# Kernel tuning notes

Hardware: AMD Instinct MI355X
Metric: run time of the kernel (lower is better)

The kernel has to match this reference:

```python
import jax, jax.numpy as jnp
import numpy as np

DIM = 128
HEAD_K = 4
EXPAND = DIM * HEAD_K  # 512
B, H, W = 16, 32, 32


def setup_inputs() -> dict:
    key = jax.random.key(0)
    ks = jax.random.split(key, 6)
    s = 0.05
    return {
        "x": jax.random.normal(ks[0], (B, DIM, H, W), dtype=jnp.float32),
        "Wq": jax.random.normal(ks[1], (EXPAND, DIM), dtype=jnp.float32) * s,
        "Wk": jax.random.normal(ks[2], (EXPAND, DIM), dtype=jnp.float32) * s,
        "Wv": jax.random.normal(ks[3], (EXPAND, DIM), dtype=jnp.float32) * s,
        "bv": jnp.zeros((EXPAND,), dtype=jnp.float32),
        "Wt": jax.random.normal(ks[4], (DIM, EXPAND), dtype=jnp.float32) * s,
        "bt": jnp.zeros((DIM,), dtype=jnp.float32),
    }


def reference(x, Wq, Wk, Wv, bv, Wt, bt):
    b, c, h, w = x.shape
    hw = h * w
    norm = jnp.asarray(c ** 0.5, x.dtype)
    xf = x.reshape(b, c, hw)  # 1x1 conv == channel matmul
    # [B, expand, HW] -> [B, head_k, dim, HW]
    q = jnp.einsum('oc,bcn->bon', Wq, xf).reshape(b, HEAD_K, DIM, hw)
    k = jnp.einsum('oc,bcn->bon', Wk, xf).reshape(b, HEAD_K, DIM, hw)
    v = (jnp.einsum('oc,bcn->bon', Wv, xf) + bv[None, :, None]).reshape(b, HEAD_K, DIM, hw)
    # score: [B, head_k, HW, HW]
    score = jax.nn.softmax(jnp.einsum('bhdn,bhdm->bhnm', q, k) / norm, axis=-1)
    # weighted sum: [B, head_k, HW, dim] -> reshape (row-major) to [B, expand, H, W]
    wsv = jnp.einsum('bhnm,bhdm->bhnd', score, v).reshape(b, HEAD_K * DIM, h, w)
    # BaseConv transform: residual + 1x1 conv projection back to dim
    proj = jnp.einsum('oc,bcn->bon', Wt, wsv.reshape(b, HEAD_K * DIM, hw)) + bt[None, :, None]
    return x + proj.reshape(b, c, h, w)
```

## Files before the change

### kernel.cpp

```cpp
#include <hip/hip_runtime.h>
#include <hip/hip_bf16.h>


#define NB 16
#define CD 128
#define HWN 1024
#define NH 4
#define KVB 64

typedef __attribute__((ext_vector_type(8))) short bf16x8;
typedef __attribute__((ext_vector_type(4))) short bf16x4;
typedef __attribute__((ext_vector_type(4))) float f32x4;
typedef __attribute__((ext_vector_type(16))) float f32x16;

static __device__ __forceinline__ short f2bf(float f) {
  union { float f; unsigned u; } v; v.f = f;
  unsigned r = v.u + 0x7fffu + ((v.u >> 16) & 1u);
  return (short)(r >> 16);
}

static __device__ __forceinline__ unsigned pk2(float a, float b) {
  unsigned r;
  asm("v_cvt_pk_bf16_f32 %0, %1, %2" : "=v"(r) : "v"(a), "v"(b));
  return r;
}

static __device__ __forceinline__ bf16x4 pk4(float a0, float a1, float a2, float a3) {
  union { unsigned u[2]; bf16x4 s; } r;
  r.u[0] = pk2(a0, a1);
  r.u[1] = pk2(a2, a3);
  return r.s;
}

#define PSWAP(a, b) asm("v_permlane32_swap_b32 %0, %1" : "+v"(a), "+v"(b))

static __device__ __forceinline__ float xswap32(float x, int lane) {
  union { float f; unsigned u; } a, b;
  a.f = x; b.f = x;
  PSWAP(a.u, b.u);
  return (lane < 32) ? b.f : a.f;
}

__global__ void prep(const float* __restrict__ x, const float* __restrict__ Wq,
                     const float* __restrict__ Wk, const float* __restrict__ Wv,
                     const float* __restrict__ Wt,
                     short* __restrict__ wqkv, short* __restrict__ wtb,
                     short* __restrict__ xt) {
  __shared__ short tile[32][33];
  if (blockIdx.z == 16) {
    const float SC = 0.08838834764831845f * 1.44269504088896341f;
    int gid = (blockIdx.x * 4 + blockIdx.y) * 256 + threadIdx.x;
#pragma unroll
    for (int t = 0; t < 2; ++t) {
      int i = gid + t * 32768;
      wqkv[i]          = f2bf(Wq[i] * SC);
      wqkv[i + 65536]  = f2bf(Wk[i]);
      wqkv[i + 131072] = f2bf(Wv[i]);
      wtb[i]           = f2bf(Wt[i]);
    }
    return;
  }
  int b = blockIdx.z, c0 = blockIdx.y * 32, n0 = blockIdx.x * 32;
  int tx = threadIdx.x & 31, ty = threadIdx.x >> 5;
  const float* xp = x + ((size_t)b * CD + c0) * HWN + n0;
  for (int k = 0; k < 4; ++k)
    tile[ty + 8 * k][tx] = f2bf(xp[(size_t)(ty + 8 * k) * HWN + tx]);
  __syncthreads();
  short* xo = xt + ((size_t)b * HWN + n0) * CD + c0;
  for (int k = 0; k < 4; ++k)
    xo[(size_t)(ty + 8 * k) * CD + tx] = tile[tx][ty + 8 * k];
}

__launch_bounds__(256)
__global__ void qkv_gemm(const short* __restrict__ wqkv, const short* __restrict__ xt,
                         const float* __restrict__ bv,
                         short* __restrict__ Qt, short* __restrict__ Kt,
                         short* __restrict__ Vd) {
  int b = blockIdx.z;
  int wave = threadIdx.x >> 6, lane = threadIdx.x & 63;
  int l15 = lane & 15, l4 = lane >> 4;
  int o0 = blockIdx.y * 128 + wave * 32;
  int n0 = blockIdx.x * 128;
  bool isV = (blockIdx.y >= 8);

  bf16x8 afrag[2][4];
  for (int of = 0; of < 2; ++of)
    for (int kt = 0; kt < 4; ++kt)
      afrag[of][kt] = *(const bf16x8*)(wqkv + (size_t)(o0 + of * 16 + l15) * CD + kt * 32 + l4 * 8);

  f32x4 acc[2][8];
  for (int of = 0; of < 2; ++of)
    for (int jt = 0; jt < 8; ++jt) acc[of][jt] = (f32x4){0.f, 0.f, 0.f, 0.f};

  const short* xb = xt + (size_t)b * HWN * CD;
  if (!isV) {
    for (int jt = 0; jt < 8; ++jt) {
      int n = n0 + jt * 16 + l15;
      for (int kt = 0; kt < 4; ++kt) {
        bf16x8 bfrag = *(const bf16x8*)(xb + (size_t)n * CD + kt * 32 + l4 * 8);
        acc[0][jt] = __builtin_amdgcn_mfma_f32_16x16x32_bf16(afrag[0][kt], bfrag, acc[0][jt], 0, 0, 0);
        acc[1][jt] = __builtin_amdgcn_mfma_f32_16x16x32_bf16(afrag[1][kt], bfrag, acc[1][jt], 0, 0, 0);
      }
    }
    short* dst = (o0 < 512) ? Qt : Kt;
    int oo = (o0 < 512) ? o0 : o0 - 512;
    for (int of = 0; of < 2; ++of) {
      int h = (oo + of * 16) >> 7, d0 = ((oo + of * 16) & 127) + l4 * 4;
      for (int jt = 0; jt < 8; ++jt) {
        int n = n0 + jt * 16 + l15;
        *(bf16x4*)(dst + (((size_t)b * NH + h) * HWN + n) * CD + d0) =
            pk4(acc[of][jt][0], acc[of][jt][1], acc[of][jt][2], acc[of][jt][3]);
      }
    }
  } else {
    for (int jt = 0; jt < 8; ++jt) {
      int n = n0 + jt * 16 + l15;
      for (int kt = 0; kt < 4; ++kt) {
        bf16x8 bfrag = *(const bf16x8*)(xb + (size_t)n * CD + kt * 32 + l4 * 8);
        acc[0][jt] = __builtin_amdgcn_mfma_f32_16x16x32_bf16(bfrag, afrag[0][kt], acc[0][jt], 0, 0, 0);
        acc[1][jt] = __builtin_amdgcn_mfma_f32_16x16x32_bf16(bfrag, afrag[1][kt], acc[1][jt], 0, 0, 0);
      }
    }
    int oo = o0 - 1024;
    for (int of = 0; of < 2; ++of) {
      int h = (oo + of * 16) >> 7, dr = ((oo + of * 16) & 127) + l15;
      float bvl = bv[oo + of * 16 + l15];
      for (int jt = 0; jt < 8; ++jt) {
        *(bf16x4*)(Vd + (((size_t)b * NH + h) * CD + dr) * HWN + n0 + jt * 16 + l4 * 4) =
            pk4(acc[of][jt][0] + bvl, acc[of][jt][1] + bvl,
                acc[of][jt][2] + bvl, acc[of][jt][3] + bvl);
      }
    }
  }
}

__launch_bounds__(256, 2)
__global__ void attn(const short* __restrict__ Qt, const short* __restrict__ Kt,
                     const short* __restrict__ Vd, short* __restrict__ Oscr) {
  int wid = blockIdx.x;
  int work = (wid & 7) * 64 + (wid >> 3);
  int xb = work & 7;
  int h = (work >> 3) & 3;
  int b = work >> 5;

  int wave = threadIdx.x >> 6, lane = threadIdx.x & 63;
  int l15 = lane & 15, l4 = lane >> 4;
  int q5 = lane & 31, hi = lane >> 5;
  int n0 = xb * 128 + wave * 32;
  size_t bh = (size_t)b * NH + h;
  const short* q = Qt + bh * HWN * CD;
  const short* k = Kt + bh * HWN * CD;
  const short* v = Vd + bh * CD * HWN;

  __shared__ short Kls[2][KVB * CD];
  __shared__ short Vls[2][CD * KVB];

#define STAGE(buf, m0s)                                                         \
  for (int j = 0; j < 4; ++j) {                                                 \
    int ii = wave * 4 + j;                                                      \
    int krow = ii * 4 + l4;                                                     \
    int kcol = (l15 * 16) ^ ((krow & 7) << 4);                                  \
    const short* kgp = k + (size_t)((m0s) + krow) * CD + (kcol >> 1);           \
    __builtin_amdgcn_global_load_lds(                                           \
        (const __attribute__((address_space(1))) void*)kgp,                     \
        (__attribute__((address_space(3))) void*)&Kls[buf][ii * 512], 16, 0, 0);\
    int vrow = ii * 8 + (lane >> 3);                                            \
    int vcol = ((lane & 7) * 16) ^ ((vrow & 7) << 4);                           \
    const short* vgp = v + (size_t)vrow * HWN + (m0s) + (vcol >> 1);            \
    __builtin_amdgcn_global_load_lds(                                           \
        (const __attribute__((address_space(1))) void*)vgp,                     \
        (__attribute__((address_space(3))) void*)&Vls[buf][ii * 512], 16, 0, 0);\
  }

  bf16x8 bq[8];
  for (int kt = 0; kt < 8; ++kt)
    bq[kt] = *(const bf16x8*)(q + (size_t)(n0 + q5) * CD + kt * 16 + hi * 8);

  f32x16 oacc[4];
  for (int dt = 0; dt < 4; ++dt)
#pragma unroll
    for (int r = 0; r < 16; ++r) oacc[dt][r] = 0.f;
  float mi = -1e30f, li = 0.f;

  STAGE(0, 0)
  __syncthreads();

  for (int mt = 0; mt < 16; ++mt) {
    int m0 = mt * KVB;
    int cur = mt & 1;
    if (mt < 15) STAGE(cur ^ 1, m0 + KVB)

    f32x16 s0, s1;
#pragma unroll
    for (int r = 0; r < 16; ++r) { s0[r] = 0.f; s1[r] = 0.f; }
    __builtin_amdgcn_s_setprio(1);
#pragma unroll
    for (int kt = 0; kt < 8; ++kt) {
      int col = kt * 16 + hi * 8;
      bf16x8 ak0 = *(const bf16x8*)&Kls[cur][q5 * CD + (col ^ ((q5 & 7) << 3))];
      bf16x8 ak1 = *(const bf16x8*)&Kls[cur][(32 + q5) * CD + (col ^ ((q5 & 7) << 3))];
      s0 = __builtin_amdgcn_mfma_f32_32x32x16_bf16(ak0, bq[kt], s0, 0, 0, 0);
      s1 = __builtin_amdgcn_mfma_f32_32x32x16_bf16(ak1, bq[kt], s1, 0, 0, 0);
    }
    __builtin_amdgcn_s_setprio(0);

    float mx = s0[0];
#pragma unroll
    for (int r = 1; r < 16; ++r) mx = fmaxf(mx, s0[r]);
#pragma unroll
    for (int r = 0; r < 16; ++r) mx = fmaxf(mx, s1[r]);
    mx = fmaxf(mx, xswap32(mx, lane));

    if (!__all(mx - mi <= 8.0f)) {
      float nm = fmaxf(mi, mx);
      float fac = __builtin_amdgcn_exp2f(mi - nm);
      mi = nm;
      li *= fac;
      for (int dt = 0; dt < 4; ++dt)
#pragma unroll
        for (int r = 0; r < 16; ++r) oacc[dt][r] *= fac;
    }
    float ls = 0.f;
#pragma unroll
    for (int r = 0; r < 16; ++r) {
      float e0 = __builtin_amdgcn_exp2f(s0[r] - mi);
      float e1 = __builtin_amdgcn_exp2f(s1[r] - mi);
      s0[r] = e0; s1[r] = e1;
      ls += e0 + e1;
    }
    ls += xswap32(ls, lane);
    li += ls;

    unsigned pkw[2][4][2];
#pragma unroll
    for (int g = 0; g < 4; ++g) {
      pkw[0][g][0] = pk2(s0[4 * g + 0], s0[4 * g + 1]);
      pkw[0][g][1] = pk2(s0[4 * g + 2], s0[4 * g + 3]);
      pkw[1][g][0] = pk2(s1[4 * g + 0], s1[4 * g + 1]);
      pkw[1][g][1] = pk2(s1[4 * g + 2], s1[4 * g + 3]);
    }
    bf16x8 pb[4];
#pragma unroll
    for (int ks = 0; ks < 4; ++ks) {
      int t = ks >> 1, G0 = 2 * (ks & 1);
      unsigned a0 = pkw[t][G0][0], b0 = pkw[t][G0 + 1][0];
      unsigned a1 = pkw[t][G0][1], b1 = pkw[t][G0 + 1][1];
      PSWAP(a0, b0);
      PSWAP(a1, b1);
      union { unsigned u[4]; bf16x8 v; } f;
      f.u[0] = a0; f.u[1] = a1; f.u[2] = b0; f.u[3] = b1;
      pb[ks] = f.v;
    }

    __builtin_amdgcn_s_setprio(1);
#pragma unroll
    for (int dt = 0; dt < 4; ++dt) {
      int d = dt * 32 + q5;
      const short* vb = &Vls[cur][d * KVB];
#pragma unroll
      for (int ks = 0; ks < 4; ++ks) {
        bf16x8 av = *(const bf16x8*)&vb[(ks * 16 + hi * 8) ^ ((d & 7) << 3)];
        oacc[dt] = __builtin_amdgcn_mfma_f32_32x32x16_bf16(av, pb[ks], oacc[dt], 0, 0, 0);
      }
    }
    __builtin_amdgcn_s_setprio(0);

    __syncthreads();
  }
#undef STAGE

  float inv = 1.0f / li;
  int n = n0 + q5;
  int o = h * CD + (n >> 3);
  size_t base = ((size_t)b * HWN + (n & 7) * CD) * 512 + o;
  for (int dt = 0; dt < 4; ++dt) {
#pragma unroll
    for (int r = 0; r < 16; ++r) {
      int d = dt * 32 + (r & 3) + 8 * (r >> 2) + 4 * hi;
      Oscr[base + (size_t)d * 512] = f2bf(oacc[dt][r] * inv);
    }
  }
}

__launch_bounds__(256)
__global__ void proj_kernel(const short* __restrict__ Oscr, const short* __restrict__ wtb,
                            const float* __restrict__ bt, const float* __restrict__ x,
                            float* __restrict__ out) {
  int b = blockIdx.y;
  int wave = threadIdx.x >> 6, lane = threadIdx.x & 63;
  int l15 = lane & 15, l4 = lane >> 4;
  int m0 = blockIdx.x * 32 + (wave & 1) * 16;
  int c0 = (wave >> 1) * 64;

  f32x4 acc[4];
  for (int jt = 0; jt < 4; ++jt) acc[jt] = (f32x4){0.f, 0.f, 0.f, 0.f};

  const short* ob = Oscr + (size_t)b * HWN * 512;
  for (int kt = 0; kt < 16; ++kt) {
    bf16x8 a = *(const bf16x8*)(ob + (size_t)(m0 + l15) * 512 + kt * 32 + l4 * 8);
    for (int jt = 0; jt < 4; ++jt) {
      bf16x8 bw = *(const bf16x8*)(wtb + (size_t)(c0 + jt * 16 + l15) * 512 + kt * 32 + l4 * 8);
      acc[jt] = __builtin_amdgcn_mfma_f32_16x16x32_bf16(a, bw, acc[jt], 0, 0, 0);
    }
  }
  for (int jt = 0; jt < 4; ++jt) {
    int c = c0 + jt * 16 + l15;
    float btc = bt[c];
    size_t base = ((size_t)b * CD + c) * HWN + m0 + l4 * 4;
    f32x4 xr = *(const f32x4*)(x + base);
    f32x4 o;
    for (int r = 0; r < 4; ++r) o[r] = acc[jt][r] + xr[r] + btc;
    *(f32x4*)(out + base) = o;
  }
}

extern "C" void kernel_launch(void* const* d_in, const int* in_sizes, int n_in,
                              void* d_out, int out_size, void* d_ws, size_t ws_size,
                              hipStream_t stream) {
  const float* x  = (const float*)d_in[0];
  const float* Wq = (const float*)d_in[1];
  const float* Wk = (const float*)d_in[2];
  const float* Wv = (const float*)d_in[3];
  const float* bv = (const float*)d_in[4];
  const float* Wt = (const float*)d_in[5];
  const float* bt = (const float*)d_in[6];
  float* out = (float*)d_out;
  char* ws = (char*)d_ws;

  short* wqkv = (short*)(ws);
  short* wtb  = (short*)(ws + 393216);
  short* xt   = (short*)(ws + 524288);
  short* Qt   = (short*)(ws + 4718592);
  short* Kt   = (short*)(ws + 21495808);
  short* Vd   = (short*)(ws + 38273024);
  short* Oscr = (short*)(ws + 55050240);

  hipLaunchKernelGGL(prep, dim3(32, 4, 17), dim3(256), 0, stream, x, Wq, Wk, Wv, Wt, wqkv, wtb, xt);
  hipLaunchKernelGGL(qkv_gemm, dim3(8, 12, 16), dim3(256), 0, stream, wqkv, xt, bv, Qt, Kt, Vd);
  hipLaunchKernelGGL(attn, dim3(512), dim3(256), 0, stream, Qt, Kt, Vd, Oscr);
  hipLaunchKernelGGL(proj_kernel, dim3(32, 16), dim3(256), 0, stream, Oscr, wtb, bt, x, out);
}
```

Measured before the change: 115.7 us.

## Stage GEMM operand tiles in swizzled LDS via direct loads, remap blocks per XCD

The qkv and projection GEMMs now load their shared activation tile (xt rows or Oscr rows) once per block into XOR-swizzled LDS using global_load_lds. Before, each wave re-read those rows from global memory. Both kernels move to a 1D grid with a work remap that groups batches across the 8 XCDs to improve L2 locality. s_setprio raises priority around the MFMA loops. The cost is extra LDS per block (32 KB) and a barrier, which may limit occupancy.

Result: faster. 100.8 us (-12.9%).

```diff
diff --git a/kernel.cpp b/kernel.cpp
--- a/kernel.cpp
+++ b/kernel.cpp
@@ -76,12 +76,30 @@
                          const float* __restrict__ bv,
                          short* __restrict__ Qt, short* __restrict__ Kt,
                          short* __restrict__ Vd) {
-  int b = blockIdx.z;
+  int wid = blockIdx.x;
+  int work = (wid & 7) * 192 + (wid >> 3);
+  int b = work / 96;
+  int rem = work - b * 96;
+  int oy = rem >> 3;
+  int nx = rem & 7;
+
   int wave = threadIdx.x >> 6, lane = threadIdx.x & 63;
   int l15 = lane & 15, l4 = lane >> 4;
-  int o0 = blockIdx.y * 128 + wave * 32;
-  int n0 = blockIdx.x * 128;
-  bool isV = (blockIdx.y >= 8);
+  int o0 = oy * 128 + wave * 32;
+  int n0 = nx * 128;
+  bool isV = (oy >= 8);
+
+  __shared__ short Xls[128 * CD];
+
+  for (int j = 0; j < 8; ++j) {
+    int ii = wave * 8 + j;
+    int row = ii * 4 + l4;
+    int scol = (l15 * 16) ^ ((row & 7) << 4);
+    const short* gp = xt + ((size_t)b * HWN + n0 + row) * CD + (scol >> 1);
+    __builtin_amdgcn_global_load_lds(
+        (const __attribute__((address_space(1))) void*)gp,
+        (__attribute__((address_space(3))) void*)&Xls[ii * 512], 16, 0, 0);
+  }
 
   bf16x8 afrag[2][4];
   for (int of = 0; of < 2; ++of)
@@ -92,16 +110,19 @@
   for (int of = 0; of < 2; ++of)
     for (int jt = 0; jt < 8; ++jt) acc[of][jt] = (f32x4){0.f, 0.f, 0.f, 0.f};
 
-  const short* xb = xt + (size_t)b * HWN * CD;
+  __syncthreads();
+
   if (!isV) {
+    __builtin_amdgcn_s_setprio(1);
     for (int jt = 0; jt < 8; ++jt) {
-      int n = n0 + jt * 16 + l15;
+      int rb = (jt * 16 + l15) * CD;
       for (int kt = 0; kt < 4; ++kt) {
-        bf16x8 bfrag = *(const bf16x8*)(xb + (size_t)n * CD + kt * 32 + l4 * 8);
+        bf16x8 bfrag = *(const bf16x8*)&Xls[rb + ((kt * 32 + l4 * 8) ^ ((l15 & 7) << 3))];
         acc[0][jt] = __builtin_amdgcn_mfma_f32_16x16x32_bf16(afrag[0][kt], bfrag, acc[0][jt], 0, 0, 0);
         acc[1][jt] = __builtin_amdgcn_mfma_f32_16x16x32_bf16(afrag[1][kt], bfrag, acc[1][jt], 0, 0, 0);
       }
     }
+    __builtin_amdgcn_s_setprio(0);
     short* dst = (o0 < 512) ? Qt : Kt;
     int oo = (o0 < 512) ? o0 : o0 - 512;
     for (int of = 0; of < 2; ++of) {
@@ -113,14 +134,16 @@
       }
     }
   } else {
+    __builtin_amdgcn_s_setprio(1);
     for (int jt = 0; jt < 8; ++jt) {
-      int n = n0 + jt * 16 + l15;
+      int rb = (jt * 16 + l15) * CD;
       for (int kt = 0; kt < 4; ++kt) {
-        bf16x8 bfrag = *(const bf16x8*)(xb + (size_t)n * CD + kt * 32 + l4 * 8);
+        bf16x8 bfrag = *(const bf16x8*)&Xls[rb + ((kt * 32 + l4 * 8) ^ ((l15 & 7) << 3))];
         acc[0][jt] = __builtin_amdgcn_mfma_f32_16x16x32_bf16(bfrag, afrag[0][kt], acc[0][jt], 0, 0, 0);
         acc[1][jt] = __builtin_amdgcn_mfma_f32_16x16x32_bf16(bfrag, afrag[1][kt], acc[1][jt], 0, 0, 0);
       }
     }
+    __builtin_amdgcn_s_setprio(0);
     int oo = o0 - 1024;
     for (int of = 0; of < 2; ++of) {
       int h = (oo + of * 16) >> 7, dr = ((oo + of * 16) & 127) + l15;
@@ -286,27 +309,47 @@
 __global__ void proj_kernel(const short* __restrict__ Oscr, const short* __restrict__ wtb,
                             const float* __restrict__ bt, const float* __restrict__ x,
                             float* __restrict__ out) {
-  int b = blockIdx.y;
+  int wid = blockIdx.x;
+  int work = (wid & 7) * 64 + (wid >> 3);
+  int b = work >> 5;
+  int mx = work & 31;
+
   int wave = threadIdx.x >> 6, lane = threadIdx.x & 63;
   int l15 = lane & 15, l4 = lane >> 4;
-  int m0 = blockIdx.x * 32 + (wave & 1) * 16;
+  int m0b = mx * 32;
+  int mloc = (wave & 1) * 16;
   int c0 = (wave >> 1) * 64;
+
+  __shared__ short Ols[32 * 512];
+
+  for (int j = 0; j < 8; ++j) {
+    int row = wave * 8 + j;
+    int scol = (lane * 16) ^ ((row & 7) << 4);
+    const short* gp = Oscr + ((size_t)b * HWN + m0b + row) * 512 + (scol >> 1);
+    __builtin_amdgcn_global_load_lds(
+        (const __attribute__((address_space(1))) void*)gp,
+        (__attribute__((address_space(3))) void*)&Ols[row * 512], 16, 0, 0);
+  }
 
   f32x4 acc[4];
   for (int jt = 0; jt < 4; ++jt) acc[jt] = (f32x4){0.f, 0.f, 0.f, 0.f};
 
-  const short* ob = Oscr + (size_t)b * HWN * 512;
+  __syncthreads();
+
+  __builtin_amdgcn_s_setprio(1);
   for (int kt = 0; kt < 16; ++kt) {
-    bf16x8 a = *(const bf16x8*)(ob + (size_t)(m0 + l15) * 512 + kt * 32 + l4 * 8);
+    bf16x8 a = *(const bf16x8*)&Ols[(mloc + l15) * 512 + ((kt * 32 + l4 * 8) ^ ((l15 & 7) << 3))];
     for (int jt = 0; jt < 4; ++jt) {
       bf16x8 bw = *(const bf16x8*)(wtb + (size_t)(c0 + jt * 16 + l15) * 512 + kt * 32 + l4 * 8);
       acc[jt] = __builtin_amdgcn_mfma_f32_16x16x32_bf16(a, bw, acc[jt], 0, 0, 0);
     }
   }
+  __builtin_amdgcn_s_setprio(0);
+
   for (int jt = 0; jt < 4; ++jt) {
     int c = c0 + jt * 16 + l15;
     float btc = bt[c];
-    size_t base = ((size_t)b * CD + c) * HWN + m0 + l4 * 4;
+    size_t base = ((size_t)b * CD + c) * HWN + m0b + mloc + l4 * 4;
     f32x4 xr = *(const f32x4*)(x + base);
     f32x4 o;
     for (int r = 0; r < 4; ++r) o[r] = acc[jt][r] + xr[r] + btc;
@@ -336,7 +379,7 @@
   short* Oscr = (short*)(ws + 55050240);
 
   hipLaunchKernelGGL(prep, dim3(32, 4, 17), dim3(256), 0, stream, x, Wq, Wk, Wv, Wt, wqkv, wtb, xt);
-  hipLaunchKernelGGL(qkv_gemm, dim3(8, 12, 16), dim3(256), 0, stream, wqkv, xt, bv, Qt, Kt, Vd);
+  hipLaunchKernelGGL(qkv_gemm, dim3(1536), dim3(256), 0, stream, wqkv, xt, bv, Qt, Kt, Vd);
   hipLaunchKernelGGL(attn, dim3(512), dim3(256), 0, stream, Qt, Kt, Vd, Oscr);
-  hipLaunchKernelGGL(proj_kernel, dim3(32, 16), dim3(256), 0, stream, Oscr, wtb, bt, x, out);
-}
+  hipLaunchKernelGGL(proj_kernel, dim3(512), dim3(256), 0, stream, Oscr, wtb, bt, x, out);
+}
```
